# Kernel tuning notes

Hardware: AMD Instinct MI355X
Metric: run time of the kernel (lower is better)

Reference implementation:

```python
import jax, jax.numpy as jnp
import numpy as np

WIN = 1024          # frame_length / fft_length
HOP = 256           # frame_step
FRAMES = 1024
BATCH = 16
BINS = WIN // 2 + 1  # 513
OUTPUT_LENGTH = (FRAMES - 1) * HOP + WIN  # 262912, matches init_kwargs


def setup_inputs() -> dict:
    key = jax.random.key(0)
    k1, k2 = jax.random.split(key)
    stft_real = jax.random.normal(k1, (BATCH, FRAMES, BINS), dtype=jnp.float32)
    stft_imag = jax.random.normal(k2, (BATCH, FRAMES, BINS), dtype=jnp.float32)
    return {"stft_real": stft_real, "stft_imag": stft_imag}


def reference(stft_real, stft_imag):
    # Complex spectrogram [B, F, BINS]
    spec = jax.lax.complex(stft_real, stft_imag)
    frames = jnp.fft.irfft(spec, n=WIN, axis=-1).astype(jnp.float32)
    # Periodic Hann window (matches tf.signal.hann_window default periodic=True)
    window = 0.5 - 0.5 * jnp.cos(
        2.0 * jnp.pi * jnp.arange(WIN, dtype=jnp.float32) / WIN
    )
    frames = frames * window
    idx = jnp.arange(FRAMES)[:, None] * HOP + jnp.arange(WIN)[None, :]
    total = (FRAMES - 1) * HOP + WIN
    out = jnp.zeros((BATCH, total), dtype=jnp.float32).at[:, idx].add(frames)
    # Trim to requested output_length (tf.signal.inverse_stft semantics)
    return out[:, :OUTPUT_LENGTH]
```

## Files before the change

### kernel.cpp

```cpp
#include <hip/hip_runtime.h>
#include <math.h>

namespace {
constexpr int HOP_    = 256;
constexpr int FRAMES_ = 1024;
constexpr int BATCH_  = 16;
constexpr int BINS_   = 513;
constexpr int OUTLEN_ = 262912;
constexpr int FPB_    = 16;
constexpr int BPB_    = FRAMES_ / FPB_;
constexpr int OWN_    = FPB_ * HOP_;
constexpr int BUF_    = OWN_ + 768;
constexpr int ACCSZ_  = 5472;
constexpr int FBUF_   = 576;
}

__device__ __forceinline__ void cmul(float& xr, float& xi, float yr, float yi) {
    float tr = xr * yr - xi * yi;
    xi = xr * yi + xi * yr;
    xr = tr;
}

__device__ __forceinline__ void dft8(float (&Yr)[8], float (&Yi)[8]) {
    const float t0r = Yr[0] + Yr[4], t0i = Yi[0] + Yi[4];
    const float t1r = Yr[0] - Yr[4], t1i = Yi[0] - Yi[4];
    const float t2r = Yr[2] + Yr[6], t2i = Yi[2] + Yi[6];
    const float t3r = Yr[2] - Yr[6], t3i = Yi[2] - Yi[6];
    const float E0r = t0r + t2r, E0i = t0i + t2i;
    const float E1r = t1r - t3i, E1i = t1i + t3r;
    const float E2r = t0r - t2r, E2i = t0i - t2i;
    const float E3r = t1r + t3i, E3i = t1i - t3r;
    const float u0r = Yr[1] + Yr[5], u0i = Yi[1] + Yi[5];
    const float u1r = Yr[1] - Yr[5], u1i = Yi[1] - Yi[5];
    const float u2r = Yr[3] + Yr[7], u2i = Yi[3] + Yi[7];
    const float u3r = Yr[3] - Yr[7], u3i = Yi[3] - Yi[7];
    const float O0r = u0r + u2r, O0i = u0i + u2i;
    const float O1r = u1r - u3i, O1i = u1i + u3r;
    const float O2r = u0r - u2r, O2i = u0i - u2i;
    const float O3r = u1r + u3i, O3i = u1i - u3r;
    const float rc = 0.7071067811865476f;
    const float W1r = rc * (O1r - O1i), W1i = rc * (O1r + O1i);
    const float W2r = -O2i,             W2i = O2r;
    const float W3r = -rc * (O3r + O3i), W3i = rc * (O3r - O3i);
    Yr[0] = E0r + O0r; Yi[0] = E0i + O0i;
    Yr[4] = E0r - O0r; Yi[4] = E0i - O0i;
    Yr[1] = E1r + W1r; Yi[1] = E1i + W1i;
    Yr[5] = E1r - W1r; Yi[5] = E1i - W1i;
    Yr[2] = E2r + W2r; Yi[2] = E2i + W2i;
    Yr[6] = E2r - W2r; Yi[6] = E2i - W2i;
    Yr[3] = E3r + W3r; Yi[3] = E3i + W3i;
    Yr[7] = E3r - W3r; Yi[7] = E3i - W3i;
}

__global__ __launch_bounds__(256, 4)
void istft_r8_kernel(const float* __restrict__ sre,
                     const float* __restrict__ sim,
                     float* __restrict__ out)
{
    __shared__ float fftbuf[4 * 2 * FBUF_];
    __shared__ __align__(16) float acc[ACCSZ_];

    const int tid   = threadIdx.x;
    const int l     = tid & 63;
    const int wv    = tid >> 6;
    const int blkid = blockIdx.x;
    const int b     = blockIdx.y;
    const int F0    = blkid * FPB_;
    const int blen  = (blkid == BPB_ - 1) ? BUF_ : OWN_;

    float* Re = fftbuf + wv * (2 * FBUF_);
    float* Im = Re + FBUF_;

    for (int u = tid; u < ACCSZ_; u += 256) acc[u] = 0.0f;

    float Wkr[8], Wki[8];
    {
        float s, c; sincosf(0.006135923151542565f * (float)l, &s, &c);
        Wkr[0] = c; Wki[0] = s;
        const float pr = 0.9238795325112867f, pq = 0.3826834323650898f;
        #pragma unroll
        for (int r = 1; r < 8; ++r) {
            Wkr[r] = Wkr[r-1]; Wki[r] = Wki[r-1];
            cmul(Wkr[r], Wki[r], pr, pq);
        }
    }
    float T1r[8], T1i[8];
    {
        T1r[0] = 1.f; T1i[0] = 0.f;
        float br = Wkr[0], bi = Wki[0];
        cmul(br, bi, Wkr[0], Wki[0]);
        T1r[1] = br; T1i[1] = bi;
        #pragma unroll
        for (int r = 2; r < 8; ++r) {
            T1r[r] = T1r[r-1]; T1i[r] = T1i[r-1];
            cmul(T1r[r], T1i[r], br, bi);
        }
    }
    float T2r[8], T2i[8];
    {
        float s, c; sincosf(0.09817477042468103f * (float)(l & 7), &s, &c);
        T2r[0] = 1.f; T2i[0] = 0.f;
        T2r[1] = c;   T2i[1] = s;
        #pragma unroll
        for (int k = 2; k < 8; ++k) {
            T2r[k] = T2r[k-1]; T2i[k] = T2i[k-1];
            cmul(T2r[k], T2i[k], c, s);
        }
    }
    const int c_ = ((l & 7) << 3) + (l >> 3);
    float we[8], wo[8];
    {
        float sf, cf; sincosf(0.012271846303085130f * (float)c_, &sf, &cf);
        const float C2 = 0.9999811752826011f, S2 = 0.006135884649154475f;
        const float rc = 0.7071067811865476f;
        const float cw[8] = {1.f, rc, 0.f, -rc, -1.f, -rc, 0.f, rc};
        const float sw[8] = {0.f, rc, 1.f, rc, 0.f, -rc, -1.f, -rc};
        #pragma unroll
        for (int w = 0; w < 8; ++w) {
            const float ct = cw[w] * cf - sw[w] * sf;
            const float st = sw[w] * cf + cw[w] * sf;
            we[w] = 0.5f - 0.5f * ct;
            wo[w] = 0.5f - 0.5f * (ct * C2 - st * S2);
        }
    }

    __syncthreads();

    const float cs = 1.0f / 1024.0f;
    const int d = l >> 3, u = l & 7;
    const int sk1 = l + (l >> 3);
    const int sk2 = 72 * d + u;
    const int sk3 = 9 * l;

    #pragma unroll 1
    for (int t = 0; t < 5; ++t) {
        const int fi = wv * 5 + t - 3;
        const int f  = F0 + fi;
        if (fi <= 15 && f >= 0) {
            const size_t base = ((size_t)b * FRAMES_ + f) * BINS_;

            float Yr[8], Yi[8];
            #pragma unroll
            for (int r = 0; r < 8; ++r) {
                const int k = l + 64 * r;
                float ar = sre[base + k];
                float ai = sim[base + k];
                float br = sre[base + 512 - k];
                float bi = -sim[base + 512 - k];
                if (r == 0 && l == 0) { ai = 0.f; bi = 0.f; }
                const float er = (ar + br) * cs, ei = (ai + bi) * cs;
                const float dr = (ar - br) * cs, di = (ai - bi) * cs;
                const float orr = Wkr[r] * dr - Wki[r] * di;
                const float oii = Wkr[r] * di + Wki[r] * dr;
                Yr[r] = er - oii;
                Yi[r] = ei + orr;
            }

            dft8(Yr, Yi);
            #pragma unroll
            for (int r = 1; r < 8; ++r) cmul(Yr[r], Yi[r], T1r[r], T1i[r]);
            #pragma unroll
            for (int r = 0; r < 8; ++r) {
                Re[sk1 + 72 * r] = Yr[r];
                Im[sk1 + 72 * r] = Yi[r];
            }

            #pragma unroll
            for (int v = 0; v < 8; ++v) {
                Yr[v] = Re[sk2 + 9 * v];
                Yi[v] = Im[sk2 + 9 * v];
            }
            dft8(Yr, Yi);
            #pragma unroll
            for (int s = 1; s < 8; ++s) cmul(Yr[s], Yi[s], T2r[s], T2i[s]);
            #pragma unroll
            for (int s = 0; s < 8; ++s) {
                Re[sk2 + 9 * s] = Yr[s];
                Im[sk2 + 9 * s] = Yi[s];
            }

            #pragma unroll
            for (int j = 0; j < 8; ++j) {
                Yr[j] = Re[sk3 + j];
                Yi[j] = Im[sk3 + j];
            }
            dft8(Yr, Yi);

            const int p0 = fi * HOP_ + 2 * c_;
            #pragma unroll
            for (int w = 0; w < 8; ++w) {
                const int pos = p0 + 128 * w;
                if ((unsigned)pos < (unsigned)blen) {
                    const int q = pos + 2 * (pos >> 4);
                    float2* ap = reinterpret_cast<float2*>(&acc[q]);
                    float2 v = *ap;
                    v.x += Yr[w] * we[w];
                    v.y += Yi[w] * wo[w];
                    *ap = v;
                }
            }
        }
        __syncthreads();
    }

    const size_t ob = (size_t)b * OUTLEN_ + (size_t)F0 * HOP_;
    for (int s = tid; s < blen; s += 256)
        out[ob + s] = acc[s + 2 * (s >> 4)];
}

extern "C" void kernel_launch(void* const* d_in, const int* in_sizes, int n_in,
                              void* d_out, int out_size, void* d_ws, size_t ws_size,
                              hipStream_t stream)
{
    (void)in_sizes; (void)n_in; (void)d_ws; (void)ws_size; (void)out_size;
    const float* sre = (const float*)d_in[0];
    const float* sim = (const float*)d_in[1];
    float* out = (float*)d_out;

    istft_r8_kernel<<<dim3(BPB_, BATCH_), dim3(256), 0, stream>>>(sre, sim, out);
}
```

Baseline: 121.5 us.

## Prefetch next frame loads, interleave frames across waves, use LDS atomics for overlap-add

The frame-to-wave mapping changes from contiguous (wave handles frames 5w-3..) to interleaved (frames w-3+4t). Each wave also prefetches the next frame's global loads into registers while the current frame's FFT runs. Because waves now touch overlapping output ranges at the same time, the per-iteration __syncthreads is removed and shared-memory atomicAdd is used for accumulation. The FFT scratch buffer becomes interleaved float2, and the accumulator is unpadded so zeroing and the final store can use float4. The trade-offs are higher register pressure from the prefetch buffers, the cost of LDS atomics, and possible bank conflicts in the unpadded accumulator.

Result: slower. 223.8 us (+84.2%).

```diff
diff --git a/kernel.cpp b/kernel.cpp
--- a/kernel.cpp
+++ b/kernel.cpp
@@ -11,8 +11,7 @@
 constexpr int BPB_    = FRAMES_ / FPB_;
 constexpr int OWN_    = FPB_ * HOP_;
 constexpr int BUF_    = OWN_ + 768;
-constexpr int ACCSZ_  = 5472;
-constexpr int FBUF_   = 576;
+constexpr int FB2_    = 576;
 }
 
 __device__ __forceinline__ void cmul(float& xr, float& xi, float yr, float yi) {
@@ -53,12 +52,12 @@
 }
 
 __global__ __launch_bounds__(256, 4)
-void istft_r8_kernel(const float* __restrict__ sre,
-                     const float* __restrict__ sim,
-                     float* __restrict__ out)
+void istft_r8v2_kernel(const float* __restrict__ sre,
+                       const float* __restrict__ sim,
+                       float* __restrict__ out)
 {
-    __shared__ float fftbuf[4 * 2 * FBUF_];
-    __shared__ __align__(16) float acc[ACCSZ_];
+    __shared__ float2 fbuf[4][FB2_];
+    __shared__ __align__(16) float acc[BUF_];
 
     const int tid   = threadIdx.x;
     const int l     = tid & 63;
@@ -68,10 +67,13 @@
     const int F0    = blkid * FPB_;
     const int blen  = (blkid == BPB_ - 1) ? BUF_ : OWN_;
 
-    float* Re = fftbuf + wv * (2 * FBUF_);
-    float* Im = Re + FBUF_;
-
-    for (int u = tid; u < ACCSZ_; u += 256) acc[u] = 0.0f;
+    float2* fb = fbuf[wv];
+
+    {
+        float4* a4 = reinterpret_cast<float4*>(acc);
+        for (int v = tid; v < BUF_ / 4; v += 256)
+            a4[v] = make_float4(0.f, 0.f, 0.f, 0.f);
+    }
 
     float Wkr[8], Wki[8];
     {
@@ -127,26 +129,44 @@
     __syncthreads();
 
     const float cs = 1.0f / 1024.0f;
-    const int d = l >> 3, u = l & 7;
-    const int sk1 = l + (l >> 3);
-    const int sk2 = 72 * d + u;
-    const int sk3 = 9 * l;
+    const int sk1f = l + (l >> 3);
+    const int sk2f = 72 * (l >> 3) + (l & 7);
+    const int sk3f = 9 * l;
+    const int lo_fi = (blkid == 0) ? 0 : -3;
+
+    float La[8], Lb[8], Lc[8], Ld[8];
+
+    auto issue = [&](int fi) {
+        const int f = F0 + fi;
+        const size_t base = ((size_t)b * FRAMES_ + f) * BINS_;
+        #pragma unroll
+        for (int r = 0; r < 8; ++r) {
+            const int k = l + 64 * r;
+            La[r] = sre[base + k];
+            Lb[r] = sim[base + k];
+            Lc[r] = sre[base + 512 - k];
+            Ld[r] = sim[base + 512 - k];
+        }
+    };
+
+    {
+        const int fi0 = wv - 3;
+        if (fi0 >= lo_fi) issue(fi0);
+    }
 
     #pragma unroll 1
     for (int t = 0; t < 5; ++t) {
-        const int fi = wv * 5 + t - 3;
-        const int f  = F0 + fi;
-        if (fi <= 15 && f >= 0) {
-            const size_t base = ((size_t)b * FRAMES_ + f) * BINS_;
-
-            float Yr[8], Yi[8];
+        const int fi  = wv - 3 + 4 * t;
+        const bool val   = (fi >= lo_fi) && (fi <= 15);
+        const int  fin   = fi + 4;
+        const bool vnext = (t < 4) && (fin >= lo_fi) && (fin <= 15);
+
+        float Yr[8], Yi[8];
+        if (val) {
             #pragma unroll
             for (int r = 0; r < 8; ++r) {
-                const int k = l + 64 * r;
-                float ar = sre[base + k];
-                float ai = sim[base + k];
-                float br = sre[base + 512 - k];
-                float bi = -sim[base + 512 - k];
+                float ar = La[r], ai = Lb[r];
+                float br = Lc[r], bi = -Ld[r];
                 if (r == 0 && l == 0) { ai = 0.f; bi = 0.f; }
                 const float er = (ar + br) * cs, ei = (ai + bi) * cs;
                 const float dr = (ar - br) * cs, di = (ai - bi) * cs;
@@ -155,34 +175,33 @@
                 Yr[r] = er - oii;
                 Yi[r] = ei + orr;
             }
-
             dft8(Yr, Yi);
             #pragma unroll
             for (int r = 1; r < 8; ++r) cmul(Yr[r], Yi[r], T1r[r], T1i[r]);
             #pragma unroll
-            for (int r = 0; r < 8; ++r) {
-                Re[sk1 + 72 * r] = Yr[r];
-                Im[sk1 + 72 * r] = Yi[r];
-            }
-
+            for (int r = 0; r < 8; ++r)
+                fb[sk1f + 72 * r] = make_float2(Yr[r], Yi[r]);
+        }
+
+        if (vnext) issue(fin);
+
+        if (val) {
             #pragma unroll
             for (int v = 0; v < 8; ++v) {
-                Yr[v] = Re[sk2 + 9 * v];
-                Yi[v] = Im[sk2 + 9 * v];
+                const float2 p = fb[sk2f + 9 * v];
+                Yr[v] = p.x; Yi[v] = p.y;
             }
             dft8(Yr, Yi);
             #pragma unroll
             for (int s = 1; s < 8; ++s) cmul(Yr[s], Yi[s], T2r[s], T2i[s]);
             #pragma unroll
-            for (int s = 0; s < 8; ++s) {
-                Re[sk2 + 9 * s] = Yr[s];
-                Im[sk2 + 9 * s] = Yi[s];
-            }
+            for (int s = 0; s < 8; ++s)
+                fb[sk2f + 9 * s] = make_float2(Yr[s], Yi[s]);
 
             #pragma unroll
             for (int j = 0; j < 8; ++j) {
-                Yr[j] = Re[sk3 + j];
-                Yi[j] = Im[sk3 + j];
+                const float2 p = fb[sk3f + j];
+                Yr[j] = p.x; Yi[j] = p.y;
             }
             dft8(Yr, Yi);
 
@@ -191,21 +210,19 @@
             for (int w = 0; w < 8; ++w) {
                 const int pos = p0 + 128 * w;
                 if ((unsigned)pos < (unsigned)blen) {
-                    const int q = pos + 2 * (pos >> 4);
-                    float2* ap = reinterpret_cast<float2*>(&acc[q]);
-                    float2 v = *ap;
-                    v.x += Yr[w] * we[w];
-                    v.y += Yi[w] * wo[w];
-                    *ap = v;
+                    atomicAdd(&acc[pos],     Yr[w] * we[w]);
+                    atomicAdd(&acc[pos + 1], Yi[w] * wo[w]);
                 }
             }
         }
-        __syncthreads();
-    }
+    }
+
+    __syncthreads();
 
     const size_t ob = (size_t)b * OUTLEN_ + (size_t)F0 * HOP_;
-    for (int s = tid; s < blen; s += 256)
-        out[ob + s] = acc[s + 2 * (s >> 4)];
+    float4* o4 = reinterpret_cast<float4*>(out + ob);
+    const float4* a4 = reinterpret_cast<const float4*>(acc);
+    for (int v = tid; v < (blen >> 2); v += 256) o4[v] = a4[v];
 }
 
 extern "C" void kernel_launch(void* const* d_in, const int* in_sizes, int n_in,
@@ -217,5 +234,5 @@
     const float* sim = (const float*)d_in[1];
     float* out = (float*)d_out;
 
-    istft_r8_kernel<<<dim3(BPB_, BATCH_), dim3(256), 0, stream>>>(sre, sim, out);
-}
+    istft_r8v2_kernel<<<dim3(BPB_, BATCH_), dim3(256), 0, stream>>>(sre, sim, out);
+}
```
